# Performance work log

Hardware: AMD Instinct MI355X
Metric: run time of the kernel (lower is better)

The kernel has to match this reference:

```python
import jax, jax.numpy as jnp
import numpy as np
import math

D_INNER = 512
D_STATE = 16
DT_RANK = 32
B_SZ = 2
L_SEQ = 4096


def setup_inputs() -> dict:
    key = jax.random.key(0)
    ks = jax.random.split(key, 6)
    x = jax.random.normal(ks[0], (B_SZ, L_SEQ, D_INNER), dtype=jnp.float32)
    # parameters (match torch init semantics closely enough for a numeric baseline)
    A = jnp.arange(1, D_STATE + 1, dtype=jnp.float32)
    A_log = jnp.broadcast_to(jnp.log(A)[None, :], (D_INNER, D_STATE)).copy()
    D_param = jnp.ones((D_INNER,), dtype=jnp.float32)
    # x_proj: Linear(d_inner -> dt_rank + 2*d_state), no bias
    W_xproj = jax.random.normal(ks[1], (DT_RANK + 2 * D_STATE, D_INNER), dtype=jnp.float32) / np.sqrt(D_INNER)
    # dt_proj: Linear(dt_rank -> d_inner) with special bias init
    W_dt = jax.random.normal(ks[2], (D_INNER, DT_RANK), dtype=jnp.float32) / np.sqrt(DT_RANK)
    dt_init = jnp.exp(jax.random.uniform(ks[3], (D_INNER,)) * (math.log(0.1) - math.log(0.001)) + math.log(0.001))
    b_dt = jnp.log(jnp.exp(dt_init) - 1.0)
    alpha = jnp.asarray(0.6, dtype=jnp.float32)
    beta_logit = jnp.asarray(math.log(0.99 / (1.0 - 0.99 + 1e-08)), dtype=jnp.float32)
    return {"x": x, "A_log": A_log, "D_param": D_param, "W_xproj": W_xproj,
            "W_dt": W_dt, "b_dt": b_dt, "alpha": alpha, "beta_logit": beta_logit}


def _momentum_ssm(x, A_log, D_param, W_xproj, W_dt, b_dt, alpha, beta_logit):
    # x: (B, L, D)
    proj = jnp.einsum('bld,pd->blp', x, W_xproj)            # (B, L, r+2N)
    dt_in = proj[..., :DT_RANK]
    Bp = proj[..., DT_RANK:DT_RANK + D_STATE]                # (B, L, N)
    Cp = proj[..., DT_RANK + D_STATE:]                       # (B, L, N)
    dt = jax.nn.softplus(jnp.einsum('blr,dr->bld', dt_in, W_dt) + b_dt)  # (B, L, D)
    A = -jnp.exp(A_log)                                      # (D, N)
    A_bar = jnp.exp(dt[..., None] * A[None, None])           # (B, L, D, N)
    # fused B_bar * x_t: dt * Bp * x
    inp = dt[..., None] * Bp[:, :, None, :] * x[..., None]   # (B, L, D, N)
    beta = jax.nn.sigmoid(beta_logit)

    # scan over time; carry (h, v): (B, D, N)
    h0 = jnp.zeros((x.shape[0], D_INNER, D_STATE), dtype=x.dtype)
    v0 = jnp.zeros_like(h0)

    def step(carry, ts):
        h, v = carry
        a_t, inp_t, c_t = ts                                 # (B,D,N), (B,D,N), (B,N)
        v = beta * v + alpha * inp_t
        h = a_t * h + v
        y = jnp.einsum('bdn,bn->bd', h, c_t)
        return (h, v), y

    xs = (jnp.moveaxis(A_bar, 1, 0), jnp.moveaxis(inp, 1, 0), jnp.moveaxis(Cp, 1, 0))
    _, ys = jax.lax.scan(step, (h0, v0), xs)                 # ys: (L, B, D)
    y = jnp.moveaxis(ys, 0, 1)                               # (B, L, D)
    return y + D_param * x


def reference(x, A_log, D_param, W_xproj, W_dt, b_dt, alpha, beta_logit):
    return _momentum_ssm(x, A_log, D_param, W_xproj, W_dt, b_dt, alpha, beta_logit)
```

## Files before the change

### kernel.cpp

```cpp
#include <hip/hip_runtime.h>


#define D_IN 512
#define D_ST 16
#define DTR  32
#define BSZ  2
#define LSEQ 4096
#define PDIM 64
#define NCH  256
#define LCH  (LSEQ / NCH)
#define LOG2E 1.44269504f
#define LN2   0.69314718f

typedef __attribute__((ext_vector_type(8))) short short8;
typedef __attribute__((ext_vector_type(4))) float f32x4;
typedef _Float16 f16;
typedef __attribute__((ext_vector_type(8))) _Float16 f16x8;

__device__ inline float fast_exp2(float x) { return __builtin_amdgcn_exp2f(x); }
__device__ inline float fast_log2(float x) { return __builtin_amdgcn_logf(x); }

__device__ inline unsigned short bf16_rne(float f) {
  unsigned b = __float_as_uint(f);
  return (unsigned short)((b + 0x7fffu + ((b >> 16) & 1u)) >> 16);
}

__device__ inline void cvt8(const float4 u, const float4 v, short8& hi, short8& lo) {
  float f[8] = {u.x, u.y, u.z, u.w, v.x, v.y, v.z, v.w};
#pragma unroll
  for (int i = 0; i < 8; ++i) {
    unsigned short h = bf16_rne(f[i]);
    hi[i] = (short)h;
    float r = f[i] - __uint_as_float((unsigned)h << 16);
    lo[i] = (short)bf16_rne(r);
  }
}

__device__ inline void st16h(f16* p, const float* s) {
  f16 t[16];
#pragma unroll
  for (int i = 0; i < 16; ++i) t[i] = (f16)s[i];
  *(f16x8*)p = *(f16x8*)&t[0];
  *(f16x8*)(p + 8) = *(f16x8*)&t[8];
}
__device__ inline void ld16h(const f16* p, float* d) {
  f16x8 a = *(const f16x8*)p;
  f16x8 b = *(const f16x8*)(p + 8);
#pragma unroll
  for (int i = 0; i < 8; ++i) { d[i] = (float)a[i]; d[8 + i] = (float)b[i]; }
}

#define PWCHK(val, n)                                                        \
  pw = pw && (fabsf((val) - (float)((n) + 1) * a0) <=                        \
              2e-5f * fabsf((float)((n) + 1) * a0));

__device__ inline bool detectA2(const float* __restrict__ A_log, int d, float& a0) {
  const float4* ap = (const float4*)(A_log + (size_t)d * D_ST);
  float4 r0 = ap[0], r1 = ap[1], r2 = ap[2], r3 = ap[3];
  float4 e0 = make_float4(-__expf(r0.x) * LOG2E, -__expf(r0.y) * LOG2E,
                          -__expf(r0.z) * LOG2E, -__expf(r0.w) * LOG2E);
  float4 e1 = make_float4(-__expf(r1.x) * LOG2E, -__expf(r1.y) * LOG2E,
                          -__expf(r1.z) * LOG2E, -__expf(r1.w) * LOG2E);
  float4 e2 = make_float4(-__expf(r2.x) * LOG2E, -__expf(r2.y) * LOG2E,
                          -__expf(r2.z) * LOG2E, -__expf(r2.w) * LOG2E);
  float4 e3 = make_float4(-__expf(r3.x) * LOG2E, -__expf(r3.y) * LOG2E,
                          -__expf(r3.z) * LOG2E, -__expf(r3.w) * LOG2E);
  a0 = e0.x;
  bool pw = true;
  PWCHK(e0.y, 1) PWCHK(e0.z, 2) PWCHK(e0.w, 3)
  PWCHK(e1.x, 4) PWCHK(e1.y, 5) PWCHK(e1.z, 6) PWCHK(e1.w, 7)
  PWCHK(e2.x, 8) PWCHK(e2.y, 9) PWCHK(e2.z, 10) PWCHK(e2.w, 11)
  PWCHK(e3.x, 12) PWCHK(e3.y, 13) PWCHK(e3.z, 14) PWCHK(e3.w, 15)
  return pw;
}

#define MM3(ACC, AH, AL, BH, BL)                                        \
  ACC = __builtin_amdgcn_mfma_f32_16x16x32_bf16(AL, BH, ACC, 0, 0, 0);  \
  ACC = __builtin_amdgcn_mfma_f32_16x16x32_bf16(AH, BL, ACC, 0, 0, 0);  \
  ACC = __builtin_amdgcn_mfma_f32_16x16x32_bf16(AH, BH, ACC, 0, 0, 0);

#define LOADBF(P, S)                                          \
  {                                                           \
    const int kb = (S) * 32;                                  \
    float4 a0 = *(const float4*)(wr + kb);                    \
    float4 b0 = *(const float4*)(wr + kb + 4);                \
    float4 a1 = *(const float4*)(wr + 8192 + kb);             \
    float4 b1 = *(const float4*)(wr + 8192 + kb + 4);         \
    float4 a2 = *(const float4*)(wr + 16384 + kb);            \
    float4 b2 = *(const float4*)(wr + 16384 + kb + 4);        \
    float4 a3 = *(const float4*)(wr + 24576 + kb);            \
    float4 b3 = *(const float4*)(wr + 24576 + kb + 4);        \
    cvt8(a0, b0, P##h0, P##l0);                               \
    cvt8(a1, b1, P##h1, P##l1);                               \
    cvt8(a2, b2, P##h2, P##l2);                               \
    cvt8(a3, b3, P##h3, P##l3);                               \
  }

#define LOADA(Aa, Ab, S)                              \
  {                                                   \
    const int ka = (S) * 32;                          \
    Aa = *(const float4*)(xr + ka);                   \
    Ab = *(const float4*)(xr + ka + 4);               \
  }

#define COMPSTEP(Aa, Ab, P)                           \
  {                                                   \
    short8 ahi, alo;                                  \
    cvt8(Aa, Ab, ahi, alo);                           \
    MM3(acc0, ahi, alo, P##h0, P##l0);                \
    MM3(acc1, ahi, alo, P##h1, P##l1);                \
    MM3(acc2, ahi, alo, P##h2, P##l2);                \
    MM3(acc3, ahi, alo, P##h3, P##l3);                \
  }

__global__ __launch_bounds__(256) void k_proj(const float* __restrict__ x,
                                              const float* __restrict__ W,
                                              float* __restrict__ proj) {
  __shared__ float Pacc[4][16][64];
  const int row0 = blockIdx.x * 16;
  const int l = threadIdx.x & 63;
  const int wq = threadIdx.x >> 6;
  const int m = l & 15;
  const int ko = (l >> 4) * 8 + wq * 128;
  const float* xr = x + (size_t)(row0 + m) * D_IN + ko;
  const float* wr = W + (size_t)m * D_IN + ko;

  f32x4 acc0 = {0.f, 0.f, 0.f, 0.f}, acc1 = acc0, acc2 = acc0, acc3 = acc0;
  float4 A0a, A0b, A1a, A1b, A2a, A2b, A3a, A3b;
  short8 Xh0, Xh1, Xh2, Xh3, Xl0, Xl1, Xl2, Xl3;
  short8 Yh0, Yh1, Yh2, Yh3, Yl0, Yl1, Yl2, Yl3;
  LOADA(A0a, A0b, 0); LOADA(A1a, A1b, 1); LOADA(A2a, A2b, 2); LOADA(A3a, A3b, 3);
  LOADBF(X, 0); LOADBF(Y, 1);

  COMPSTEP(A0a, A0b, X); LOADBF(X, 2);
  COMPSTEP(A1a, A1b, Y); LOADBF(Y, 3);
  COMPSTEP(A2a, A2b, X);
  COMPSTEP(A3a, A3b, Y);

  const int r0 = (l >> 4) * 4;
#pragma unroll
  for (int r = 0; r < 4; ++r) {
    Pacc[wq][r0 + r][m] = acc0[r];
    Pacc[wq][r0 + r][16 + m] = acc1[r];
    Pacc[wq][r0 + r][32 + m] = acc2[r];
    Pacc[wq][r0 + r][48 + m] = acc3[r];
  }
  __syncthreads();

  const int orow = threadIdx.x >> 4;
  const int ocol = (threadIdx.x & 15) * 4;
  float4 s0 = *(const float4*)&Pacc[0][orow][ocol];
  float4 s1 = *(const float4*)&Pacc[1][orow][ocol];
  float4 s2 = *(const float4*)&Pacc[2][orow][ocol];
  float4 s3 = *(const float4*)&Pacc[3][orow][ocol];
  float4 o = make_float4((s0.x + s1.x) + (s2.x + s3.x), (s0.y + s1.y) + (s2.y + s3.y),
                         (s0.z + s1.z) + (s2.z + s3.z), (s0.w + s1.w) + (s2.w + s3.w));
  *(float4*)(proj + (size_t)(row0 + orow) * PDIM + ocol) = o;
}

#define S1_LOOP                                                              \
  _Pragma("unroll")                                                          \
  for (int j = 0; j < LCH; ++j) {                                            \
    const float4* pj = (const float4*)(pb + j * PDIM);                       \
    float4 pp[8];                                                            \
    _Pragma("unroll")                                                        \
    for (int k = 0; k < 8; ++k) pp[k] = pj[k];                               \
    float c0 = bb, c1 = 0.f, c2 = 0.f, c3 = 0.f;                             \
    _Pragma("unroll")                                                        \
    for (int k = 0; k < 8; ++k) {                                            \
      c0 = fmaf(pp[k].x, w4[k].x, c0);                                       \
      c1 = fmaf(pp[k].y, w4[k].y, c1);                                       \
      c2 = fmaf(pp[k].z, w4[k].z, c2);                                       \
      c3 = fmaf(pp[k].w, w4[k].w, c3);                                       \
    }                                                                        \
    const float acc = (c0 + c1) + (c2 + c3);                                 \
    const float ee = fast_exp2(acc * LOG2E);                                 \
    const float dtc = (acc > 20.f) ? acc : LN2 * fast_log2(1.f + ee);        \
    dp[(size_t)j * D_IN] = (f16)dtc;                                         \
    sd += dtc;                                                               \
    bpow *= beta;                                                            \
    const float u = alpha * dtc * xs[j];                                     \
    float4 bq[4];                                                            \
    _Pragma("unroll")                                                        \
    for (int k = 0; k < 4; ++k) bq[k] = pj[8 + k];                           \
    const float* Bf = (const float*)bq;                                      \
    AR_INIT;                                                                 \
    _Pragma("unroll")                                                        \
    for (int n = 0; n < 16; ++n) {                                           \
      AR_STEP;                                                               \
      v[n] = fmaf(beta, v[n], u * Bf[n]);                                    \
      h[n] = fmaf(ar, h[n], v[n]);                                           \
      cv[n] = fmaf(ar, cv[n], bpow);                                         \
    }                                                                        \
  }

__global__ __launch_bounds__(256) void k_scan1(const float* __restrict__ x,
                                               const float* __restrict__ proj,
                                               const float* __restrict__ A_log,
                                               const float* __restrict__ W_dt,
                                               const float* __restrict__ b_dt,
                                               const float* __restrict__ alpha_p,
                                               const float* __restrict__ beta_p,
                                               f16* __restrict__ hh,
                                               f16* __restrict__ vh,
                                               f16* __restrict__ cvv,
                                               float* __restrict__ sdt,
                                               f16* __restrict__ dth) {
  const int c = blockIdx.x, b = blockIdx.z;
  const int d = blockIdx.y * 256 + threadIdx.x;
  const int t0 = c * LCH;
  const float* pb = proj + ((size_t)b * LSEQ + t0) * PDIM;

  float xs[LCH];
  {
    const float* xp = x + ((size_t)b * LSEQ + t0) * D_IN + d;
#pragma unroll
    for (int j = 0; j < LCH; ++j) xs[j] = xp[(size_t)j * D_IN];
  }
  float4 w4[8];
  {
    const float4* wp = (const float4*)(W_dt + (size_t)d * DTR);
#pragma unroll
    for (int i = 0; i < 8; ++i) w4[i] = wp[i];
  }
  const float bb = b_dt[d];
  const float alpha = alpha_p[0];
  const float beta = 1.f / (1.f + __expf(-beta_p[0]));
  float a0;
  const bool pw = detectA2(A_log, d, a0);

  f16* dp = dth + ((size_t)b * LSEQ + t0) * D_IN + d;
  float h[16] = {}, v[16] = {}, cv[16] = {};
  float bpow = 1.f, sd = 0.f;

  if (pw) {
#define AR_INIT const float r = fast_exp2(dtc * a0); float ar = 1.f
#define AR_STEP ar *= r
    S1_LOOP
#undef AR_INIT
#undef AR_STEP
  } else {
    volatile const float* av = A_log + (size_t)d * D_ST;
#define AR_INIT float ar
#define AR_STEP ar = fast_exp2(dtc * (-__expf(av[n]) * LOG2E))
    S1_LOOP
#undef AR_INIT
#undef AR_STEP
  }

  const size_t base = ((size_t)(b * NCH + c) * D_IN + d) * D_ST;
  st16h(hh + base, h);
  st16h(vh + base, v);
  st16h(cvv + base, cv);
  sdt[(size_t)(b * NCH + c) * D_IN + d] = sd;
}

__global__ __launch_bounds__(256) void k_fix(f16* __restrict__ hh,
                                             f16* __restrict__ vh,
                                             const f16* __restrict__ cvv,
                                             const float* __restrict__ sdt,
                                             const float* __restrict__ A_log,
                                             const float* __restrict__ beta_p) {
  const int lane = threadIdx.x & 63;
  const int wv = threadIdx.x >> 6;
  const int span = lane & 15;
  const int g = blockIdx.x * 16 + wv * 4 + (lane >> 4);
  const int b = g >> 13;
  const int dn = g & 8191;
  const float beta = 1.f / (1.f + __expf(-beta_p[0]));
  const float A2 = -__expf(A_log[dn]) * LOG2E;
  float bL = beta;
#pragma unroll
  for (int i = 0; i < 4; ++i) bL *= bL;

  const size_t cs = (size_t)D_IN * D_ST;
  const int c0 = span * 16;
  const size_t base = (size_t)b * NCH * cs + dn;
  const size_t sbase = (size_t)b * NCH * D_IN + (dn >> 4);

  float hc[16], vc[16], cvc[16], Pa[16];
#pragma unroll
  for (int i = 0; i < 16; ++i) {
    const int c = c0 + i;
    hc[i] = (float)hh[base + (size_t)c * cs];
    vc[i] = (float)vh[base + (size_t)c * cs];
    cvc[i] = (float)cvv[base + (size_t)c * cs];
    Pa[i] = fast_exp2(sdt[sbase + (size_t)c * D_IN] * A2);
  }
  float SP = 1.f, Sq = 0.f, Sh = 0.f, Sv = 0.f, Sw = 1.f;
#pragma unroll
  for (int i = 0; i < 16; ++i) {
    Sq = fmaf(Pa[i], Sq, cvc[i] * Sw);
    Sh = fmaf(Pa[i], Sh, fmaf(cvc[i], Sv, hc[i]));
    SP = Pa[i] * SP;
    Sv = fmaf(bL, Sv, vc[i]);
    Sw = bL * Sw;
  }

#pragma unroll
  for (int s = 1; s < 16; s <<= 1) {
    float AP = __shfl_up(SP, s, 16);
    float Aq = __shfl_up(Sq, s, 16);
    float Ah = __shfl_up(Sh, s, 16);
    float Av = __shfl_up(Sv, s, 16);
    float Aw = __shfl_up(Sw, s, 16);
    if (span >= s) {
      const float nP = SP * AP;
      const float nq = fmaf(SP, Aq, Sq * Aw);
      const float nh = fmaf(SP, Ah, fmaf(Sq, Av, Sh));
      const float nv = fmaf(Sw, Av, Sv);
      const float nw = Sw * Aw;
      SP = nP; Sq = nq; Sh = nh; Sv = nv; Sw = nw;
    }
  }

  float H = __shfl_up(Sh, 1, 16);
  float V = __shfl_up(Sv, 1, 16);
  if (span == 0) { H = 0.f; V = 0.f; }

#pragma unroll
  for (int i = 0; i < 16; ++i) {
    const int c = c0 + i;
    hh[base + (size_t)c * cs] = (f16)H;
    vh[base + (size_t)c * cs] = (f16)V;
    const float Hn = fmaf(Pa[i], H, fmaf(cvc[i], V, hc[i]));
    V = fmaf(bL, V, vc[i]);
    H = Hn;
  }
}

#define S2_LOOP                                                              \
  _Pragma("unroll")                                                          \
  for (int j = 0; j < LCH; ++j) {                                            \
    const float4* pj = (const float4*)(pb + j * PDIM);                       \
    float4 bq[8];                                                            \
    _Pragma("unroll")                                                        \
    for (int k = 0; k < 8; ++k) bq[k] = pj[8 + k];                           \
    const float* Bf = (const float*)bq;                                      \
    const float dtc = dtv[j], xv = xs[j];                                    \
    const float u = alpha * dtc * xv;                                        \
    float y0 = 0.f, y1 = 0.f, y2 = 0.f, y3 = 0.f;                            \
    AR_INIT;                                                                 \
    _Pragma("unroll")                                                        \
    for (int n = 0; n < 16; ++n) {                                           \
      AR_STEP;                                                               \
      v[n] = fmaf(beta, v[n], u * Bf[n]);                                    \
      h[n] = fmaf(ar, h[n], v[n]);                                           \
      float hc = h[n] * Bf[16 + n];                                          \
      if ((n & 3) == 0) y0 += hc;                                            \
      else if ((n & 3) == 1) y1 += hc;                                       \
      else if ((n & 3) == 2) y2 += hc;                                       \
      else y3 += hc;                                                         \
    }                                                                        \
    op[(size_t)j * D_IN] = (y0 + y1) + (y2 + y3) + Dv * xv;                  \
  }

__global__ __launch_bounds__(256) void k_scan2(const float* __restrict__ x,
                                               const f16* __restrict__ dth,
                                               const float* __restrict__ proj,
                                               const float* __restrict__ A_log,
                                               const float* __restrict__ D_param,
                                               const float* __restrict__ alpha_p,
                                               const float* __restrict__ beta_p,
                                               const f16* __restrict__ hh,
                                               const f16* __restrict__ vh,
                                               float* __restrict__ out) {
  const int c = blockIdx.x, b = blockIdx.z;
  const int d = blockIdx.y * 256 + threadIdx.x;
  const int t0 = c * LCH;
  const float* pb = proj + ((size_t)b * LSEQ + t0) * PDIM;

  float xs[LCH], dtv[LCH];
  {
    const float* xp = x + ((size_t)b * LSEQ + t0) * D_IN + d;
    const f16* dp = dth + ((size_t)b * LSEQ + t0) * D_IN + d;
#pragma unroll
    for (int j = 0; j < LCH; ++j) xs[j] = xp[(size_t)j * D_IN];
#pragma unroll
    for (int j = 0; j < LCH; ++j) dtv[j] = (float)dp[(size_t)j * D_IN];
  }
  const float alpha = alpha_p[0];
  const float beta = 1.f / (1.f + __expf(-beta_p[0]));
  const float Dv = D_param[d];
  float a0;
  const bool pw = detectA2(A_log, d, a0);
  const size_t ibase = ((size_t)(b * NCH + c) * D_IN + d) * D_ST;
  float h[16], v[16];
  ld16h(hh + ibase, h);
  ld16h(vh + ibase, v);

  float* op = out + ((size_t)b * LSEQ + t0) * D_IN + d;
  if (pw) {
#define AR_INIT const float r = fast_exp2(dtc * a0); float ar = 1.f
#define AR_STEP ar *= r
    S2_LOOP
#undef AR_INIT
#undef AR_STEP
  } else {
    volatile const float* av = A_log + (size_t)d * D_ST;
#define AR_INIT float ar
#define AR_STEP ar = fast_exp2(dtc * (-__expf(av[n]) * LOG2E))
    S2_LOOP
#undef AR_INIT
#undef AR_STEP
  }
}

extern "C" void kernel_launch(void* const* d_in, const int* in_sizes, int n_in,
                              void* d_out, int out_size, void* d_ws, size_t ws_size,
                              hipStream_t stream) {
  const float* x = (const float*)d_in[0];
  const float* A_log = (const float*)d_in[1];
  const float* D_param = (const float*)d_in[2];
  const float* W_xproj = (const float*)d_in[3];
  const float* W_dt = (const float*)d_in[4];
  const float* b_dt = (const float*)d_in[5];
  const float* alpha = (const float*)d_in[6];
  const float* beta_logit = (const float*)d_in[7];
  float* out = (float*)d_out;

  const size_t NST = (size_t)BSZ * NCH * D_IN * D_ST;
  float* ws = (float*)d_ws;
  float* proj = ws;
  float* sdt = proj + (size_t)BSZ * LSEQ * PDIM;
  f16* hh = (f16*)(sdt + (size_t)BSZ * NCH * D_IN);
  f16* vh = hh + NST;
  f16* cvv = vh + NST;
  f16* dth = cvv + NST;

  k_proj<<<dim3(BSZ * LSEQ / 16), dim3(256), 0, stream>>>(x, W_xproj, proj);
  k_scan1<<<dim3(NCH, D_IN / 256, BSZ), dim3(256), 0, stream>>>(
      x, proj, A_log, W_dt, b_dt, alpha, beta_logit, hh, vh, cvv, sdt, dth);
  k_fix<<<dim3(BSZ * D_IN * D_ST / 16), dim3(256), 0, stream>>>(hh, vh, cvv, sdt, A_log,
                                                                beta_logit);
  k_scan2<<<dim3(NCH, D_IN / 256, BSZ), dim3(256), 0, stream>>>(
      x, dth, proj, A_log, D_param, alpha, beta_logit, hh, vh, out);
}
```

Measured before the change: 192.0 us.

## Remap k_fix so lanes span channels and combine chunk segments via LDS

Reorganizes the chunk-carry fix-up kernel so each lane handles one (batch, d, n) channel and each wave handles 16 consecutive chunks, with 1024-thread blocks. Global loads across lanes now hit contiguous channel addresses, which coalesces the strided fp16 state accesses. The 16-way shuffle-based parallel prefix over segments is replaced by writing segment summaries to shared memory and having each wave sequentially combine its predecessors. This adds a block barrier and up to 15 serial combine steps per wave, and shrinks the grid to 256 large blocks.

Measured after the change: 156.5 us (median of 4 runs). 18.5% less time.

```diff
diff --git a/kernel.cpp b/kernel.cpp
--- a/kernel.cpp
+++ b/kernel.cpp
@@ -255,16 +255,16 @@
   sdt[(size_t)(b * NCH + c) * D_IN + d] = sd;
 }
 
-__global__ __launch_bounds__(256) void k_fix(f16* __restrict__ hh,
-                                             f16* __restrict__ vh,
-                                             const f16* __restrict__ cvv,
-                                             const float* __restrict__ sdt,
-                                             const float* __restrict__ A_log,
-                                             const float* __restrict__ beta_p) {
+__global__ __launch_bounds__(1024) void k_fix(f16* __restrict__ hh,
+                                              f16* __restrict__ vh,
+                                              const f16* __restrict__ cvv,
+                                              const float* __restrict__ sdt,
+                                              const float* __restrict__ A_log,
+                                              const float* __restrict__ beta_p) {
+  __shared__ float M[16][5][64];
   const int lane = threadIdx.x & 63;
-  const int wv = threadIdx.x >> 6;
-  const int span = lane & 15;
-  const int g = blockIdx.x * 16 + wv * 4 + (lane >> 4);
+  const int w = threadIdx.x >> 6;
+  const int g = blockIdx.x * 64 + lane;
   const int b = g >> 13;
   const int dn = g & 8191;
   const float beta = 1.f / (1.f + __expf(-beta_p[0]));
@@ -274,9 +274,9 @@
   for (int i = 0; i < 4; ++i) bL *= bL;
 
   const size_t cs = (size_t)D_IN * D_ST;
-  const int c0 = span * 16;
   const size_t base = (size_t)b * NCH * cs + dn;
   const size_t sbase = (size_t)b * NCH * D_IN + (dn >> 4);
+  const int c0 = w * 16;
 
   float hc[16], vc[16], cvc[16], Pa[16];
 #pragma unroll
@@ -296,27 +296,18 @@
     Sv = fmaf(bL, Sv, vc[i]);
     Sw = bL * Sw;
   }
-
-#pragma unroll
-  for (int s = 1; s < 16; s <<= 1) {
-    float AP = __shfl_up(SP, s, 16);
-    float Aq = __shfl_up(Sq, s, 16);
-    float Ah = __shfl_up(Sh, s, 16);
-    float Av = __shfl_up(Sv, s, 16);
-    float Aw = __shfl_up(Sw, s, 16);
-    if (span >= s) {
-      const float nP = SP * AP;
-      const float nq = fmaf(SP, Aq, Sq * Aw);
-      const float nh = fmaf(SP, Ah, fmaf(Sq, Av, Sh));
-      const float nv = fmaf(Sw, Av, Sv);
-      const float nw = Sw * Aw;
-      SP = nP; Sq = nq; Sh = nh; Sv = nv; Sw = nw;
-    }
-  }
-
-  float H = __shfl_up(Sh, 1, 16);
-  float V = __shfl_up(Sv, 1, 16);
-  if (span == 0) { H = 0.f; V = 0.f; }
+  M[w][0][lane] = SP; M[w][1][lane] = Sq; M[w][2][lane] = Sh;
+  M[w][3][lane] = Sv; M[w][4][lane] = Sw;
+  __syncthreads();
+
+  float H = 0.f, V = 0.f;
+  for (int s = 0; s < w; ++s) {
+    const float P = M[s][0][lane], q = M[s][1][lane], h = M[s][2][lane];
+    const float vv = M[s][3][lane], ww = M[s][4][lane];
+    const float Hn = fmaf(P, H, fmaf(q, V, h));
+    V = fmaf(ww, V, vv);
+    H = Hn;
+  }
 
 #pragma unroll
   for (int i = 0; i < 16; ++i) {
@@ -431,8 +422,8 @@
   k_proj<<<dim3(BSZ * LSEQ / 16), dim3(256), 0, stream>>>(x, W_xproj, proj);
   k_scan1<<<dim3(NCH, D_IN / 256, BSZ), dim3(256), 0, stream>>>(
       x, proj, A_log, W_dt, b_dt, alpha, beta_logit, hh, vh, cvv, sdt, dth);
-  k_fix<<<dim3(BSZ * D_IN * D_ST / 16), dim3(256), 0, stream>>>(hh, vh, cvv, sdt, A_log,
-                                                                beta_logit);
+  k_fix<<<dim3(BSZ * D_IN * D_ST / 64), dim3(1024), 0, stream>>>(hh, vh, cvv, sdt,
+                                                                 A_log, beta_logit);
   k_scan2<<<dim3(NCH, D_IN / 256, BSZ), dim3(256), 0, stream>>>(
       x, dth, proj, A_log, D_param, alpha, beta_logit, hh, vh, out);
 }
```
